# Performance work log

Measured on AMD Instinct MI355X. Metric: run time of the kernel, lower is better.

The kernel has to match this reference:

```python
import jax, jax.numpy as jnp
import numpy as np

VX, VY, VT = 3.0, 3.0, 1.0
PCX, PCY, PCT = 346.0, 260.0, 200.0
GX, GY = 116, 87  # ceil(346/3), ceil(260/3)
B = 4
NSEG = B * GX * GY  # dense pillar id space (replaces torch.unique)
EPS = 1e-3  # BatchNorm1d eps


def _bn_swish(h, gamma, beta):
    # BatchNorm1d (training-mode batch stats) + Swish
    mu = jnp.mean(h, axis=0)
    var = jnp.var(h, axis=0)
    h = (h - mu) * jax.lax.rsqrt(var + EPS) * gamma + beta
    return h * jax.nn.sigmoid(h)


def _voxelize(points):
    # points: [N,5] = (batch_idx, x, y, t, polarity)
    cx = jnp.floor(points[:, 1] / VX).astype(jnp.int32)
    cy = jnp.floor(points[:, 2] / VY).astype(jnp.int32)
    bi = points[:, 0].astype(jnp.int32)
    inv = (bi * GX + cx) * GY + cy  # dense pillar id == unq_inv into dense grid
    xyz = points[:, 1:4]
    cnt = jax.ops.segment_sum(jnp.ones_like(xyz[:, 0]), inv, num_segments=NSEG)
    mean = jax.ops.segment_sum(xyz, inv, num_segments=NSEG) / jnp.maximum(cnt, 1.0)[:, None]
    f_cluster = xyz - mean[inv]
    cxy = jnp.stack([cx, cy], axis=1).astype(points.dtype)
    vsz = jnp.array([VX, VY], points.dtype)
    f_center = points[:, 1:3] - (cxy * vsz + (vsz - 1.0) / 2.0)
    feats = jnp.concatenate([points[:, 1:5], f_cluster, f_center], axis=1)  # [N,9]
    scale = jnp.array([PCX, PCY, PCT, 1.0, VX, VY, PCT, VX, VY], points.dtype)
    feats = feats / scale
    return feats[:, :4], inv, cnt  # module only keeps first 4 feature columns


def _resize_bilinear_ac(x, Ho, Wo):
    # F.interpolate(mode='bilinear', align_corners=True)
    _, _, H, W = x.shape
    ys = jnp.linspace(0.0, H - 1.0, Ho)
    xs = jnp.linspace(0.0, W - 1.0, Wo)
    y0 = jnp.floor(ys).astype(jnp.int32); y1 = jnp.minimum(y0 + 1, H - 1)
    x0 = jnp.floor(xs).astype(jnp.int32); x1 = jnp.minimum(x0 + 1, W - 1)
    wy = (ys - y0.astype(x.dtype))[None, None, :, None]
    wx = (xs - x0.astype(x.dtype))[None, None, None, :]
    xh = x[:, :, y0, :] * (1.0 - wy) + x[:, :, y1, :] * wy
    return xh[:, :, :, x0] * (1.0 - wx) + xh[:, :, :, x1] * wx


def setup_inputs() -> dict:
    key = jax.random.key(0)
    ks = jax.random.split(key, 8)
    N = 1_000_000
    b = jax.random.randint(ks[0], (N, 1), 0, B).astype(jnp.float32)
    x = jax.random.uniform(ks[1], (N, 1)) * 345.9
    y = jax.random.uniform(ks[2], (N, 1)) * 259.9
    t = jax.random.uniform(ks[3], (N, 1)) * 199.9
    p = jax.random.randint(ks[4], (N, 1), 0, 2).astype(jnp.float32)
    points = jnp.concatenate([b, x, y, t, p], axis=1)
    fus = jax.random.normal(ks[5], (B, 3, 224, 224), jnp.float32)
    W0 = jax.random.normal(ks[6], (4, 32), jnp.float32) * 0.1
    g0 = jnp.ones(32, jnp.float32); b0 = jnp.zeros(32, jnp.float32)
    W1 = jax.random.normal(ks[7], (64, 128), jnp.float32) * 0.05
    g1 = jnp.ones(128, jnp.float32); b1 = jnp.zeros(128, jnp.float32)
    return {"fus": fus, "points": points, "W0": W0, "g0": g0, "b0": b0,
            "W1": W1, "g1": g1, "b1": b1}


def reference(fus, points, W0, g0, b0, W1, g1, b1):
    feats, inv, cnt = _voxelize(points)
    # PFNLayer 0 (not last): units = 64//2 = 32, concat per-pillar max
    h0 = _bn_swish(feats @ W0, g0, b0)
    m0 = jax.ops.segment_max(h0, inv, num_segments=NSEG)
    x1 = jnp.concatenate([h0, m0[inv]], axis=1)  # [N,64]
    # PFNLayer 1 (last): units = 128, returns broadcast per-pillar max
    h1 = _bn_swish(x1 @ W1, g1, b1)
    m1 = jax.ops.segment_max(h1, inv, num_segments=NSEG)  # [NSEG,128]
    # final scatter_max over the broadcast max equals m1 on occupied pillars;
    # spconv .dense() zero-fills empty pillars
    occ = cnt > 0
    dense = jnp.where(occ[:, None], m1, 0.0)
    dense = dense.reshape(B, GX, GY, -1).transpose(0, 3, 2, 1)  # [B,C,GY,GX]
    return _resize_bilinear_ac(dense, 224, 224)
```

## Files before the change

kernel.cpp:

```cpp
#include <hip/hip_runtime.h>
#include <cmath>

#define NPTS   1000000
#define GXD    116
#define GYD    87
#define NB     4
#define NSEG   40368
#define OUTN   25690112

#define OFF_INV    0
#define OFF_CNT    2000000
#define OFF_OFFS   2050000
#define OFF_FILL   2100000
#define OFF_STATS  2150000
#define OFF_BN0    2158500
#define OFF_COEF   2158600
#define OFF_FRAG   2158900
#define OFF_MINP   2170000
#define OFF_MAXP   7340000
#define OFF_SPTS   12510000

typedef __attribute__((ext_vector_type(8))) short short8v;
typedef __attribute__((ext_vector_type(4))) float float4v;

union Frag {
  unsigned u[4];
  int4 i4;
  short8v v;
};

__device__ __forceinline__ float fastrcp(float x) { return __builtin_amdgcn_rcpf(x); }
__device__ __forceinline__ float swishf(float z) { return z * fastrcp(1.0f + __expf(-z)); }
__device__ __forceinline__ unsigned fbits(float x) { return __builtin_bit_cast(unsigned, x); }
__device__ __forceinline__ float ubf(unsigned x) { return __builtin_bit_cast(float, x); }

__device__ __forceinline__ float min3f(float a, float b, float c) {
  float d; asm("v_min3_f32 %0, %1, %2, %3" : "=v"(d) : "v"(a), "v"(b), "v"(c)); return d;
}
__device__ __forceinline__ float max3f(float a, float b, float c) {
  float d; asm("v_max3_f32 %0, %1, %2, %3" : "=v"(d) : "v"(a), "v"(b), "v"(c)); return d;
}

__device__ __forceinline__ void bfsplit2(float x0, float x1, unsigned& hi, unsigned& lo) {
  unsigned h0b = fbits(x0) & 0xffff0000u;
  unsigned h1b = fbits(x1) & 0xffff0000u;
  hi = (h0b >> 16) | h1b;
  float l0 = x0 - ubf(h0b), l1 = x1 - ubf(h1b);
  lo = (fbits(l0) >> 16) | (fbits(l1) & 0xffff0000u);
}

__global__ __launch_bounds__(256) void k_init(int* __restrict__ cnt, int* __restrict__ fill,
                                              float* __restrict__ stats) {
  int i = blockIdx.x * 256 + threadIdx.x;
  if (i < NSEG) { cnt[i] = 0; fill[i] = 0; }
  if (i < 8224) stats[i] = 0.0f;
}

__global__ __launch_bounds__(256) void k_point1(const float* __restrict__ pts,
                                                int* __restrict__ inv,
                                                int* __restrict__ cnt,
                                                float* __restrict__ Sg) {
  float acc[14];
  #pragma unroll
  for (int q = 0; q < 14; ++q) acc[q] = 0.0f;
  const float i346 = 1.0f / 346.0f, i260 = 1.0f / 260.0f, i200 = 1.0f / 200.0f;
  const int stride = gridDim.x * 256;
  for (int i = blockIdx.x * 256 + threadIdx.x; i < NPTS; i += stride) {
    float b = pts[i*5];
    float4 v = *(const float4*)(pts + i*5 + 1);
    float x = v.x, y = v.y, t = v.z, p = v.w;
    int cx = (int)floorf(x / 3.0f);
    int cy = (int)floorf(y / 3.0f);
    int bi = (int)b;
    if (cx >= 0 && cx < GXD && cy >= 0 && cy < GYD && bi >= 0 && bi < NB) {
      int iv = (bi*GXD + cx)*GYD + cy;
      inv[i] = iv;
      atomicAdd(&cnt[iv], 1);
    } else {
      inv[i] = -1;
    }
    float f0 = x*i346, f1 = y*i260, f2 = t*i200, f3 = p;
    acc[0]+=f0; acc[1]+=f1; acc[2]+=f2; acc[3]+=f3;
    acc[4]+=f0*f0; acc[5]+=f0*f1; acc[6]+=f0*f2; acc[7]+=f0*f3;
    acc[8]+=f1*f1; acc[9]+=f1*f2; acc[10]+=f1*f3;
    acc[11]+=f2*f2; acc[12]+=f2*f3; acc[13]+=f3*f3;
  }
  __shared__ float lds[4*14];
  int lane = threadIdx.x & 63, wave = threadIdx.x >> 6;
  #pragma unroll
  for (int q = 0; q < 14; ++q) {
    float v = acc[q];
    #pragma unroll
    for (int d = 32; d > 0; d >>= 1) v += __shfl_down(v, d, 64);
    if (lane == 0) lds[wave*14 + q] = v;
  }
  __syncthreads();
  if (threadIdx.x < 14) {
    float v = lds[threadIdx.x] + lds[14+threadIdx.x] + lds[28+threadIdx.x] + lds[42+threadIdx.x];
    atomicAdd(&Sg[threadIdx.x], v);
  }
}

__global__ __launch_bounds__(1024) void k_scan(const int* __restrict__ cnt,
                                               int* __restrict__ offs,
                                               const float* __restrict__ S,
                                               float* __restrict__ bn0,
                                               float* __restrict__ coef,
                                               int4* __restrict__ frag,
                                               const float* __restrict__ W0,
                                               const float* __restrict__ g0,
                                               const float* __restrict__ b0,
                                               const float* __restrict__ W1) {
  __shared__ int wtot[16];
  const int tid = threadIdx.x;
  if (tid < 32) {
    const float invN = 1.0f / (float)NPTS;
    const float i346 = 1.0f/346.0f, i260 = 1.0f/260.0f, i200 = 1.0f/200.0f;
    float w0 = W0[tid], w1 = W0[32+tid], w2 = W0[64+tid], w3 = W0[96+tid];
    float mu = (S[0]*w0 + S[1]*w1 + S[2]*w2 + S[3]*w3) * invN;
    float e2 = (S[4]*w0*w0 + S[8]*w1*w1 + S[11]*w2*w2 + S[13]*w3*w3
              + 2.0f*(S[5]*w0*w1 + S[6]*w0*w2 + S[7]*w0*w3
                    + S[9]*w1*w2 + S[10]*w1*w3 + S[12]*w2*w3)) * invN;
    float var = e2 - mu*mu;
    float a = rsqrtf(var + 1e-3f) * g0[tid];
    bn0[tid] = a;
    bn0[32+tid] = b0[tid] - mu*a;
    coef[tid]        = w0 * (i346 * a);
    coef[32 + tid]   = w1 * (i260 * a);
    coef[64 + tid]   = w2 * (i200 * a);
    coef[96 + tid]   = w3 * a;
    coef[128 + tid]  = b0[tid] - mu*a;
  }
  if (tid < 512) {
    const int t = tid >> 6, ln = tid & 63;
    const int qq = ln >> 4, rr = ln & 15;
    Frag fh, fl, gh, gl;
    #pragma unroll
    for (int d = 0; d < 4; ++d) {
      int row = 8*qq + 2*d, col = 16*t + rr;
      bfsplit2(W1[row*128 + col],      W1[(row+1)*128 + col],  fh.u[d], fl.u[d]);
      bfsplit2(W1[(32+row)*128 + col], W1[(33+row)*128 + col], gh.u[d], gl.u[d]);
    }
    frag[tid]        = fh.i4;
    frag[512 + tid]  = fl.i4;
    frag[1024 + tid] = gh.i4;
    frag[1536 + tid] = gl.i4;
  }
  const int CH = 40;
  const int base = tid * CH;
  int loc[CH];
  int s = 0;
  #pragma unroll
  for (int i = 0; i < CH; ++i) {
    int v = (base + i < NSEG) ? cnt[base + i] : 0;
    loc[i] = s; s += v;
  }
  int inc = s;
  const int lane = tid & 63, wv = tid >> 6;
  #pragma unroll
  for (int d = 1; d < 64; d <<= 1) {
    int t = __shfl_up(inc, d, 64);
    if (lane >= d) inc += t;
  }
  if (lane == 63) wtot[wv] = inc;
  __syncthreads();
  if (tid == 0) {
    int run = 0;
    #pragma unroll
    for (int w = 0; w < 16; ++w) { int t = wtot[w]; wtot[w] = run; run += t; }
    offs[NSEG] = run;
  }
  __syncthreads();
  int ex = wtot[wv] + (inc - s);
  #pragma unroll
  for (int i = 0; i < CH; ++i)
    if (base + i < NSEG) offs[base + i] = ex + loc[i];
}

__global__ __launch_bounds__(256) void k_scatter(const float* __restrict__ pts,
                                                 const int* __restrict__ inv,
                                                 const int* __restrict__ offs,
                                                 int* __restrict__ fill,
                                                 float4* __restrict__ sp) {
  int i = blockIdx.x * 256 + threadIdx.x;
  if (i >= NPTS) return;
  int iv = inv[i];
  if (iv < 0) return;
  float4 v = *(const float4*)(pts + i*5 + 1);
  int pos = offs[iv] + atomicAdd(&fill[iv], 1);
  sp[pos] = v;
}

__global__ __launch_bounds__(256) void k_seg(const float4* __restrict__ sp,
                                             const int* __restrict__ offs,
                                             const float* __restrict__ coef,
                                             const int4* __restrict__ frags,
                                             float* __restrict__ minp,
                                             float* __restrict__ maxp,
                                             float* __restrict__ stats) {
  __shared__ int4 fragLDS[1536];
  __shared__ float redS[4][16][16];
  const int tid = threadIdx.x;
  const int wave = tid >> 6, lane = tid & 63;
  const int q = lane >> 4, r = lane & 15;

  short8v Bhi[8];
  #pragma unroll
  for (int t = 0; t < 8; ++t) {
    Frag f; f.i4 = frags[t*64 + lane];
    Bhi[t] = f.v;
  }
  for (int i = tid; i < 1536; i += 256) fragLDS[i] = frags[512 + i];

  const float4* cf = (const float4*)coef;
  float wax[8], way[8], wat[8], wap[8], wc0[8];
  {
    float4 a0v = cf[0*8 + 2*q], a1v = cf[0*8 + 2*q + 1];
    float4 b0v = cf[1*8 + 2*q], b1v = cf[1*8 + 2*q + 1];
    float4 c0v = cf[2*8 + 2*q], c1v = cf[2*8 + 2*q + 1];
    float4 d0v = cf[3*8 + 2*q], d1v = cf[3*8 + 2*q + 1];
    float4 e0v = cf[4*8 + 2*q], e1v = cf[4*8 + 2*q + 1];
    wax[0]=a0v.x; wax[1]=a0v.y; wax[2]=a0v.z; wax[3]=a0v.w;
    wax[4]=a1v.x; wax[5]=a1v.y; wax[6]=a1v.z; wax[7]=a1v.w;
    way[0]=b0v.x; way[1]=b0v.y; way[2]=b0v.z; way[3]=b0v.w;
    way[4]=b1v.x; way[5]=b1v.y; way[6]=b1v.z; way[7]=b1v.w;
    wat[0]=c0v.x; wat[1]=c0v.y; wat[2]=c0v.z; wat[3]=c0v.w;
    wat[4]=c1v.x; wat[5]=c1v.y; wat[6]=c1v.z; wat[7]=c1v.w;
    wap[0]=d0v.x; wap[1]=d0v.y; wap[2]=d0v.z; wap[3]=d0v.w;
    wap[4]=d1v.x; wap[5]=d1v.y; wap[6]=d1v.z; wap[7]=d1v.w;
    wc0[0]=e0v.x; wc0[1]=e0v.y; wc0[2]=e0v.z; wc0[3]=e0v.w;
    wc0[4]=e1v.x; wc0[5]=e1v.y; wc0[6]=e1v.z; wc0[7]=e1v.w;
  }
  __syncthreads();

  float gsum[8], gssq[8];
  #pragma unroll
  for (int t = 0; t < 8; ++t) { gsum[t] = 0.f; gssq[t] = 0.f; }

  const int w = blockIdx.x*4 + wave;
  const int qn = NSEG >> 13;
  const int rm = NSEG - (qn << 13);
  const int s0 = w*qn + (w < rm ? w : rm);
  const int scnt = qn + (w < rm ? 1 : 0);

  for (int s = s0; s < s0 + scnt; ++s) {
    const int off = offs[s], pend = offs[s+1];
    const int n = pend - off;
    if (n <= 0) continue;
    const int ngroups = (n + 15) >> 4;
    float m0r[8], mn[8], mx[8], su[8], sq[8];
    #pragma unroll
    for (int t = 0; t < 8; ++t) {
      m0r[t] = -1e30f; mn[t] = 1e30f; mx[t] = -1e30f; su[t] = 0.f; sq[t] = 0.f;
    }
    float4 P = sp[off + (r < n ? r : 0)];
    for (int g = 0; g < ngroups; ++g) {
      int slot1 = (g+1)*16 + r;
      float4 Pn = sp[off + (slot1 < n ? slot1 : 0)];

      float h0v[8];
      #pragma unroll
      for (int j = 0; j < 8; ++j) {
        float pre = fmaf(P.x, wax[j], fmaf(P.y, way[j], fmaf(P.z, wat[j], fmaf(P.w, wap[j], wc0[j]))));
        float h = swishf(pre);
        h0v[j] = h;
        m0r[j] = fmaxf(m0r[j], h);
      }
      Frag ah, al;
      #pragma unroll
      for (int d = 0; d < 4; ++d)
        bfsplit2(h0v[2*d], h0v[2*d+1], ah.u[d], al.u[d]);

      const int rem = n - g*16;
      __builtin_amdgcn_s_setprio(1);
      #pragma unroll
      for (int t = 0; t < 8; ++t) {
        Frag fb; fb.i4 = fragLDS[t*64 + lane];
        float4v acc = {0.f, 0.f, 0.f, 0.f};
        acc = __builtin_amdgcn_mfma_f32_16x16x32_bf16(ah.v, Bhi[t], acc, 0, 0, 0);
        acc = __builtin_amdgcn_mfma_f32_16x16x32_bf16(ah.v, fb.v,   acc, 0, 0, 0);
        acc = __builtin_amdgcn_mfma_f32_16x16x32_bf16(al.v, Bhi[t], acc, 0, 0, 0);
        float z0 = acc[0], z1 = acc[1], z2 = acc[2], z3 = acc[3];
        if (rem >= 16) {
          mn[t] = min3f(z0, z1, min3f(z2, z3, mn[t]));
          mx[t] = max3f(z0, z1, max3f(z2, z3, mx[t]));
          su[t] += (z0 + z1) + (z2 + z3);
          sq[t] = fmaf(z0, z0, sq[t]); sq[t] = fmaf(z1, z1, sq[t]);
          sq[t] = fmaf(z2, z2, sq[t]); sq[t] = fmaf(z3, z3, sq[t]);
        } else {
          mn[t] = min3f(z0, z1, min3f(z2, z3, mn[t]));
          mx[t] = max3f(z0, z1, max3f(z2, z3, mx[t]));
          float zz0 = (4*q + 0 < rem) ? z0 : 0.f;
          float zz1 = (4*q + 1 < rem) ? z1 : 0.f;
          float zz2 = (4*q + 2 < rem) ? z2 : 0.f;
          float zz3 = (4*q + 3 < rem) ? z3 : 0.f;
          su[t] += (zz0 + zz1) + (zz2 + zz3);
          sq[t] = fmaf(zz0, zz0, sq[t]); sq[t] = fmaf(zz1, zz1, sq[t]);
          sq[t] = fmaf(zz2, zz2, sq[t]); sq[t] = fmaf(zz3, zz3, sq[t]);
        }
      }
      __builtin_amdgcn_s_setprio(0);
      P = Pn;
    }

    #pragma unroll
    for (int j = 0; j < 8; ++j) {
      float v = m0r[j];
      v = fmaxf(v, __shfl_xor(v, 1, 64));
      v = fmaxf(v, __shfl_xor(v, 2, 64));
      v = fmaxf(v, __shfl_xor(v, 4, 64));
      v = fmaxf(v, __shfl_xor(v, 8, 64));
      m0r[j] = v;
    }
    Frag mh, ml;
    #pragma unroll
    for (int d = 0; d < 4; ++d)
      bfsplit2(m0r[2*d], m0r[2*d+1], mh.u[d], ml.u[d]);
    float c[8];
    #pragma unroll
    for (int t = 0; t < 8; ++t) {
      Frag gh; gh.i4 = fragLDS[512 + t*64 + lane];
      Frag gl; gl.i4 = fragLDS[1024 + t*64 + lane];
      float4v cacc = {0.f, 0.f, 0.f, 0.f};
      cacc = __builtin_amdgcn_mfma_f32_16x16x32_bf16(mh.v, gh.v, cacc, 0, 0, 0);
      cacc = __builtin_amdgcn_mfma_f32_16x16x32_bf16(mh.v, gl.v, cacc, 0, 0, 0);
      cacc = __builtin_amdgcn_mfma_f32_16x16x32_bf16(ml.v, gh.v, cacc, 0, 0, 0);
      c[t] = cacc[0];
    }
    #pragma unroll
    for (int t = 0; t < 8; ++t) {
      mn[t] = fminf(mn[t], __shfl_xor(mn[t], 16, 64));
      mn[t] = fminf(mn[t], __shfl_xor(mn[t], 32, 64));
      mx[t] = fmaxf(mx[t], __shfl_xor(mx[t], 16, 64));
      mx[t] = fmaxf(mx[t], __shfl_xor(mx[t], 32, 64));
      su[t] += __shfl_xor(su[t], 16, 64);
      su[t] += __shfl_xor(su[t], 32, 64);
      sq[t] += __shfl_xor(sq[t], 16, 64);
      sq[t] += __shfl_xor(sq[t], 32, 64);
      float nf = (float)n;
      gsum[t] += su[t] + nf * c[t];
      gssq[t] += sq[t] + 2.0f*c[t]*su[t] + nf*c[t]*c[t];
    }
    if (lane < 16) {
      #pragma unroll
      for (int t = 0; t < 8; ++t) {
        minp[(16*t + r)*NSEG + s] = mn[t] + c[t];
        maxp[(16*t + r)*NSEG + s] = mx[t] + c[t];
      }
    }
  }
  if (lane < 16) {
    #pragma unroll
    for (int t = 0; t < 8; ++t) {
      redS[wave][r][t]     = gsum[t];
      redS[wave][r][8 + t] = gssq[t];
    }
  }
  __syncthreads();
  if (wave == 0 && lane < 16) {
    const int cpy = blockIdx.x & 15;
    float* sb = stats + 16 + 512*cpy;
    #pragma unroll
    for (int t = 0; t < 8; ++t) {
      float s0v = redS[0][r][t]   + redS[1][r][t]   + redS[2][r][t]   + redS[3][r][t];
      float q0v = redS[0][r][8+t] + redS[1][r][8+t] + redS[2][r][8+t] + redS[3][r][8+t];
      atomicAdd(&sb[16*t + r], s0v);
      atomicAdd(&sb[256 + 16*t + r], q0v);
    }
  }
}

__global__ __launch_bounds__(256) void k_plane(const float* __restrict__ minp,
                                               const float* __restrict__ maxp,
                                               const int* __restrict__ offs,
                                               const float* __restrict__ stats,
                                               const float* __restrict__ g1,
                                               const float* __restrict__ b1,
                                               float* __restrict__ out) {
  __shared__ float plane[87*117];
  __shared__ float ab[2];
  const int c = blockIdx.x & 127;
  const int b = blockIdx.x >> 7;
  const int tid = threadIdx.x;
  if (tid == 0) {
    float s = 0.f, q2 = 0.f;
    #pragma unroll
    for (int cpy = 0; cpy < 16; ++cpy) {
      s  += stats[16 + 512*cpy + c];
      q2 += stats[16 + 512*cpy + 256 + c];
    }
    const float invN = 1.0f / (float)NPTS;
    float mu = s * invN;
    float var = q2 * invN - mu*mu;
    float a = rsqrtf(var + 1e-3f) * g1[c];
    ab[0] = a;
    ab[1] = b1[c] - mu*a;
  }
  __syncthreads();
  const float a = ab[0], bb = ab[1];
  const int sBase = b * (GXD*GYD);
  const float* mnp = minp + c*NSEG + sBase;
  const float* mxp = maxp + c*NSEG + sBase;
  for (int i = tid; i < GXD*GYD; i += 256) {
    int gx = i / GYD, gy = i - gx*GYD;
    float m = 0.0f;
    int s = sBase + i;
    if (offs[s+1] - offs[s] > 0) {
      float zl = fmaf(a, mnp[i], bb);
      float zh = fmaf(a, mxp[i], bb);
      m = fmaxf(swishf(zl), swishf(zh));
    }
    plane[gy*117 + gx] = m;
  }
  __syncthreads();
  float* op = out + (size_t)blockIdx.x * (224*224);
  for (int o4 = tid; o4 < 224*56; o4 += 256) {
    int xq = o4 % 56;
    int yo = o4 / 56;
    float ys = (float)yo * (86.0f/223.0f);
    float yf = floorf(ys); int y0 = (int)yf; int y1 = min(y0+1, 86); float wy = ys - yf;
    const float* p0 = plane + y0*117;
    const float* p1 = plane + y1*117;
    float res[4];
    #pragma unroll
    for (int gph = 0; gph < 4; ++gph) {
      int xo = xq*4 + gph;
      float xs = (float)xo * (115.0f/223.0f);
      float xf = floorf(xs); int x0 = (int)xf; int x1 = min(x0+1, 115); float wx = xs - xf;
      float c0v = p0[x0]*(1.0f-wy) + p1[x0]*wy;
      float c1v = p0[x1]*(1.0f-wy) + p1[x1]*wy;
      res[gph] = c0v*(1.0f-wx) + c1v*wx;
    }
    *(float4*)&op[yo*224 + xq*4] = make_float4(res[0], res[1], res[2], res[3]);
  }
}

extern "C" void kernel_launch(void* const* d_in, const int* in_sizes, int n_in,
                              void* d_out, int out_size, void* d_ws, size_t ws_size,
                              hipStream_t stream) {
  const float* pts = (const float*)d_in[1];
  const float* W0  = (const float*)d_in[2];
  const float* g0  = (const float*)d_in[3];
  const float* b0  = (const float*)d_in[4];
  const float* W1  = (const float*)d_in[5];
  const float* g1  = (const float*)d_in[6];
  const float* b1  = (const float*)d_in[7];
  float* out = (float*)d_out;
  int*   wsi = (int*)d_ws;
  float* wsf = (float*)d_ws;

  k_init<<<158, 256, 0, stream>>>(wsi+OFF_CNT, wsi+OFF_FILL, wsf+OFF_STATS);
  k_point1<<<256, 256, 0, stream>>>(pts, wsi+OFF_INV, wsi+OFF_CNT, wsf+OFF_STATS);
  k_scan<<<1, 1024, 0, stream>>>(wsi+OFF_CNT, wsi+OFF_OFFS, wsf+OFF_STATS, wsf+OFF_BN0,
                                 wsf+OFF_COEF, (int4*)(wsf+OFF_FRAG), W0, g0, b0, W1);
  k_scatter<<<(NPTS+255)/256, 256, 0, stream>>>(pts, wsi+OFF_INV, wsi+OFF_OFFS,
                                                wsi+OFF_FILL, (float4*)(wsf+OFF_SPTS));
  k_seg<<<2048, 256, 0, stream>>>((const float4*)(wsf+OFF_SPTS), wsi+OFF_OFFS,
                                  wsf+OFF_COEF, (const int4*)(wsf+OFF_FRAG),
                                  wsf+OFF_MINP, wsf+OFF_MAXP, wsf+OFF_STATS);
  k_plane<<<NB*128, 256, 0, stream>>>(wsf+OFF_MINP, wsf+OFF_MAXP, wsi+OFF_OFFS,
                                      wsf+OFF_STATS, g1, b1, out);
}
```

Measured before the change: 434.3 us.

## Split plane kernel into row bands and move B fragments from registers to LDS

```diff
diff --git a/kernel.cpp b/kernel.cpp
--- a/kernel.cpp
+++ b/kernel.cpp
@@ -198,19 +198,13 @@
                                              float* __restrict__ minp,
                                              float* __restrict__ maxp,
                                              float* __restrict__ stats) {
-  __shared__ int4 fragLDS[1536];
+  __shared__ int4 fragLDS[1024];
   __shared__ float redS[4][16][16];
   const int tid = threadIdx.x;
   const int wave = tid >> 6, lane = tid & 63;
   const int q = lane >> 4, r = lane & 15;
 
-  short8v Bhi[8];
-  #pragma unroll
-  for (int t = 0; t < 8; ++t) {
-    Frag f; f.i4 = frags[t*64 + lane];
-    Bhi[t] = f.v;
-  }
-  for (int i = tid; i < 1536; i += 256) fragLDS[i] = frags[512 + i];
+  for (int i = tid; i < 1024; i += 256) fragLDS[i] = frags[i];
 
   const float4* cf = (const float4*)coef;
   float wax[8], way[8], wat[8], wap[8], wc0[8];
@@ -275,11 +269,12 @@
       __builtin_amdgcn_s_setprio(1);
       #pragma unroll
       for (int t = 0; t < 8; ++t) {
-        Frag fb; fb.i4 = fragLDS[t*64 + lane];
+        Frag bh; bh.i4 = fragLDS[t*64 + lane];
+        Frag bl; bl.i4 = fragLDS[512 + t*64 + lane];
         float4v acc = {0.f, 0.f, 0.f, 0.f};
-        acc = __builtin_amdgcn_mfma_f32_16x16x32_bf16(ah.v, Bhi[t], acc, 0, 0, 0);
-        acc = __builtin_amdgcn_mfma_f32_16x16x32_bf16(ah.v, fb.v,   acc, 0, 0, 0);
-        acc = __builtin_amdgcn_mfma_f32_16x16x32_bf16(al.v, Bhi[t], acc, 0, 0, 0);
+        acc = __builtin_amdgcn_mfma_f32_16x16x32_bf16(ah.v, bh.v, acc, 0, 0, 0);
+        acc = __builtin_amdgcn_mfma_f32_16x16x32_bf16(ah.v, bl.v, acc, 0, 0, 0);
+        acc = __builtin_amdgcn_mfma_f32_16x16x32_bf16(al.v, bh.v, acc, 0, 0, 0);
         float z0 = acc[0], z1 = acc[1], z2 = acc[2], z3 = acc[3];
         if (rem >= 16) {
           mn[t] = min3f(z0, z1, min3f(z2, z3, mn[t]));
@@ -319,8 +314,8 @@
     float c[8];
     #pragma unroll
     for (int t = 0; t < 8; ++t) {
-      Frag gh; gh.i4 = fragLDS[512 + t*64 + lane];
-      Frag gl; gl.i4 = fragLDS[1024 + t*64 + lane];
+      Frag gh; gh.i4 = frags[1024 + t*64 + lane];
+      Frag gl; gl.i4 = frags[1536 + t*64 + lane];
       float4v cacc = {0.f, 0.f, 0.f, 0.f};
       cacc = __builtin_amdgcn_mfma_f32_16x16x32_bf16(mh.v, gh.v, cacc, 0, 0, 0);
       cacc = __builtin_amdgcn_mfma_f32_16x16x32_bf16(mh.v, gl.v, cacc, 0, 0, 0);
@@ -377,10 +372,12 @@
                                                const float* __restrict__ g1,
                                                const float* __restrict__ b1,
                                                float* __restrict__ out) {
-  __shared__ float plane[87*117];
+  __shared__ float plane[25*117];
   __shared__ float ab[2];
-  const int c = blockIdx.x & 127;
-  const int b = blockIdx.x >> 7;
+  const int pk = blockIdx.x & 3;
+  const int pl = blockIdx.x >> 2;
+  const int c = pl & 127;
+  const int b = pl >> 7;
   const int tid = threadIdx.x;
   if (tid == 0) {
     float s = 0.f, q2 = 0.f;
@@ -401,26 +398,29 @@
   const int sBase = b * (GXD*GYD);
   const float* mnp = minp + c*NSEG + sBase;
   const float* mxp = maxp + c*NSEG + sBase;
-  for (int i = tid; i < GXD*GYD; i += 256) {
-    int gx = i / GYD, gy = i - gx*GYD;
+  const int r0 = (int)floorf((float)(pk*56) * (86.0f/223.0f));
+  for (int i = tid; i < GXD*25; i += 256) {
+    int gx = i / 25, j = i - gx*25;
+    int gy = r0 + j; if (gy > 86) gy = 86;
+    int idx = gx*GYD + gy;
     float m = 0.0f;
-    int s = sBase + i;
+    int s = sBase + idx;
     if (offs[s+1] - offs[s] > 0) {
-      float zl = fmaf(a, mnp[i], bb);
-      float zh = fmaf(a, mxp[i], bb);
+      float zl = fmaf(a, mnp[idx], bb);
+      float zh = fmaf(a, mxp[idx], bb);
       m = fmaxf(swishf(zl), swishf(zh));
     }
-    plane[gy*117 + gx] = m;
-  }
-  __syncthreads();
-  float* op = out + (size_t)blockIdx.x * (224*224);
-  for (int o4 = tid; o4 < 224*56; o4 += 256) {
+    plane[j*117 + gx] = m;
+  }
+  __syncthreads();
+  float* op = out + (size_t)pl * (224*224);
+  for (int o4 = tid; o4 < 56*56; o4 += 256) {
     int xq = o4 % 56;
-    int yo = o4 / 56;
+    int yo = pk*56 + o4 / 56;
     float ys = (float)yo * (86.0f/223.0f);
     float yf = floorf(ys); int y0 = (int)yf; int y1 = min(y0+1, 86); float wy = ys - yf;
-    const float* p0 = plane + y0*117;
-    const float* p1 = plane + y1*117;
+    const float* p0 = plane + (y0 - r0)*117;
+    const float* p1 = plane + (y1 - r0)*117;
     float res[4];
     #pragma unroll
     for (int gph = 0; gph < 4; ++gph) {
@@ -458,6 +458,6 @@
   k_seg<<<2048, 256, 0, stream>>>((const float4*)(wsf+OFF_SPTS), wsi+OFF_OFFS,
                                   wsf+OFF_COEF, (const int4*)(wsf+OFF_FRAG),
                                   wsf+OFF_MINP, wsf+OFF_MAXP, wsf+OFF_STATS);
-  k_plane<<<NB*128, 256, 0, stream>>>(wsf+OFF_MINP, wsf+OFF_MAXP, wsi+OFF_OFFS,
-                                      wsf+OFF_STATS, g1, b1, out);
-}
+  k_plane<<<NB*128*4, 256, 0, stream>>>(wsf+OFF_MINP, wsf+OFF_MAXP, wsi+OFF_OFFS,
+                                        wsf+OFF_STATS, g1, b1, out);
+}
```

New measurement: 432.1 us. Within noise of the previous version (-0.5%).
